# Optimization experiments

Measured on AMD Instinct MI355X. Metric: run time of the kernel, lower is better.

## Reference

```python
import jax, jax.numpy as jnp
import numpy as np

B, S, N = 8, 4, 64
ATOM_FDIM, BOND_FDIM, H = 133, 147, 300
DEPTH = 3


def setup_inputs() -> dict:
    key = jax.random.key(0)
    ks = jax.random.split(key, 9)
    f_atoms = jax.random.normal(ks[0], (B, S, N, ATOM_FDIM), dtype=jnp.float32)
    f_bonds = jax.random.uniform(ks[1], (B, S, N, N, BOND_FDIM), dtype=jnp.float32)
    adj = (jax.random.uniform(ks[2], (B, S, N, N)) < 0.3).astype(jnp.float32)
    def lin(k, fan_in, fan_out):
        return jax.random.normal(k, (fan_in, fan_out), dtype=jnp.float32) / np.sqrt(fan_in)
    return {
        'f_atoms': f_atoms,
        'f_bonds': f_bonds,
        'adj': adj,
        'W_i_atom': lin(ks[3], ATOM_FDIM, H),   # bias=False
        'W_i_bond': lin(ks[4], BOND_FDIM, H),   # bias=False
        'W_h_0': lin(ks[5], H, H),              # bias=False
        'W_h_1': lin(ks[6], H, H),              # bias=False
        'W_o': lin(ks[7], 3 * H, H),            # bias=True
        'b_o': jax.random.normal(ks[8], (H,), dtype=jnp.float32) * 0.01,
    }


def reference(f_atoms, f_bonds, adj, W_i_atom, W_i_bond, W_h_0, W_h_1, W_o, b_o):
    act = jax.nn.relu
    # atom / bond input embeddings
    input_atom = act(f_atoms @ W_i_atom)                        # [B,S,N,H]
    message_atom = input_atom
    input_bond = act((adj[..., None] * f_bonds) @ W_i_bond)     # [B,S,N,N,H]
    message_bond = input_bond
    for W_h in (W_h_0, W_h_1):  # depth-1 message-passing steps
        agg = message_bond.sum(axis=2) * jax.nn.sigmoid(message_bond.max(axis=2))  # [B,S,N,H]
        message_atom = message_atom + agg
        resonance = jnp.einsum('bsnd,bsmd->bsnm', message_atom, message_atom) * adj  # [B,S,N,N]
        # broadcast atom messages along edges, subtract reverse message
        mb = adj[..., None] * message_atom[:, :, None, :, :] - message_bond  # [B,S,N,N,H]
        mb = jnp.swapaxes(mb, 2, 3)  # permute(0,1,3,2,4)
        mb = act(input_bond + mb @ W_h)
        message_bond = mb * jax.nn.softmax(resonance, axis=2)[..., None]
    agg = message_bond.sum(axis=2) * jax.nn.sigmoid(message_bond.max(axis=2))
    a_input = jnp.concatenate([agg, message_atom, input_atom], axis=-1)  # [B,S,N,3H]
    atom_hiddens = act(a_input @ W_o + b_o)  # [B,S,N,H]
    return atom_hiddens, message_bond
```

## Files before the change

kernel.cpp:

```cpp
#include <hip/hip_runtime.h>
#include <hip/hip_bf16.h>
#include <math.h>

#define Bc 8
#define Sc 4
#define Nc 64
#define AF 133
#define BFD 147
#define Hc 300
#define BS (Bc*Sc)
#define ROWS (BS*Nc)
#define EDGES (BS*Nc*Nc)
#define BSLICE 19456
#define BHALF  9728

typedef float f32x4 __attribute__((ext_vector_type(4)));
typedef short bf16x8 __attribute__((ext_vector_type(8)));
typedef float f32x4v __attribute__((ext_vector_type(4)));
typedef f32x4v f32x4u __attribute__((aligned(4)));
union U4 { uint4 u; bf16x8 v; };

__device__ __forceinline__ float reluf(float x){ return fmaxf(x, 0.f); }
__device__ __forceinline__ float b2f(unsigned short u){ union{unsigned int i;float f;}v; v.i = ((unsigned int)u)<<16; return v.f; }
__device__ __forceinline__ unsigned short f2b(float f){ __hip_bfloat16 h = __float2bfloat16(f); return *reinterpret_cast<unsigned short*>(&h); }
__device__ __forceinline__ void split2(float x, unsigned short &hi, unsigned short &lo){
    unsigned short h = f2b(x);
    float r = x - b2f(h);
    hi = h; lo = f2b(r);
}

typedef __attribute__((address_space(1))) const unsigned int* gas1_t;
typedef __attribute__((address_space(3))) unsigned int* las3_t;
__device__ __forceinline__ void gload_lds16(const void* g, void* l){
    __builtin_amdgcn_global_load_lds((gas1_t)g, (las3_t)l, 16, 0, 0);
}

__device__ __forceinline__ void bar_only(){
    __builtin_amdgcn_sched_barrier(0);
    asm volatile("" ::: "memory");
    __builtin_amdgcn_s_barrier();
    asm volatile("" ::: "memory");
    __builtin_amdgcn_sched_barrier(0);
}
__device__ __forceinline__ void bar_drain(){
    __builtin_amdgcn_sched_barrier(0);
    asm volatile("s_waitcnt vmcnt(0) lgkmcnt(0)" ::: "memory");
    __builtin_amdgcn_s_barrier();
    asm volatile("" ::: "memory");
    __builtin_amdgcn_sched_barrier(0);
}

__global__ __launch_bounds__(320) void k_atom_embed(const float* __restrict__ f_atoms,
        const float* __restrict__ W, float* __restrict__ input_atom, float* __restrict__ message_atom){
    __shared__ float x[AF];
    int row = blockIdx.x;
    const float* fr = f_atoms + (size_t)row*AF;
    for (int d = threadIdx.x; d < AF; d += blockDim.x) x[d] = fr[d];
    __syncthreads();
    int h = threadIdx.x;
    if (h < Hc){
        float acc = 0.f;
        for (int d = 0; d < AF; ++d) acc = fmaf(x[d], W[d*Hc + h], acc);
        float v = reluf(acc);
        input_atom[(size_t)row*Hc + h] = v;
        message_atom[(size_t)row*Hc + h] = v;
    }
}

__global__ __launch_bounds__(256) void k_prep_wp2(const float* __restrict__ W, int K, int NKT,
        unsigned short* __restrict__ WP){
    int idx = blockIdx.x*256 + threadIdx.x;
    if (idx >= NKT*BSLICE) return;
    int j  = idx & 7;
    int l  = (idx >> 3) & 63;
    int ct = (idx >> 9) % 19;
    int rem = idx / BHALF;
    int hl = rem & 1;
    int kt = rem >> 1;
    int col = ct*16 + (l & 15);
    int k   = kt*32 + (l >> 4)*8 + j;
    float v = (col < Hc && k < K) ? W[k*Hc + col] : 0.f;
    unsigned short hi, lo; split2(v, hi, lo);
    WP[idx] = hl ? lo : hi;
}

template<int MODE>
__global__ __launch_bounds__(1024) void k_gemm_t(
        const float* __restrict__ Asrc,
        const unsigned short* __restrict__ WP,
        const float* __restrict__ ma,
        const float* __restrict__ adj,
        const float* __restrict__ sm,
        const float* __restrict__ ib,
        float* __restrict__ dst)
{
    constexpr int NKT  = MODE ? 10 : 5;
    constexpr int ASTR = MODE ? 300 : BFD;

    __shared__ unsigned short sAhi[4096];
    __shared__ unsigned short sAlo[4096];
    __shared__ unsigned short sB[BSLICE];
    __shared__ int s_eOut[128];
    __shared__ int s_eRev[128];
    __shared__ float s_adjRev[128];
    __shared__ int s_aAtom[128];

    const int t = threadIdx.x;
    if (MODE){
        if (t < 128){
            int r = t;
            int bs = blockIdx.x >> 5, kk = blockIdx.x & 31;
            int s1 = 64-kk, s2 = 127-2*kk, s3 = 128-kk;
            int a, b;
            if (r < s1){ a = kk; b = kk + r; }
            else if (r < s2){ a = kk+1 + (r - s1); b = kk; }
            else if (r < s3){ a = 63-kk; b = 63-kk + (r - s2); }
            else { a = 64-kk + (r - s3); b = 63-kk; }
            int eo = (bs*64 + a)*64 + b;
            int er = (bs*64 + b)*64 + a;
            s_eOut[r] = eo; s_eRev[r] = er; s_aAtom[r] = bs*64 + a;
            s_adjRev[r] = adj[er];
        }
        __syncthreads();
    }

    const int rt_b = t >> 7;
    const int q_b  = (t >> 5) & 3;
    const int li_b = (t >> 1) & 15;
    const int half = t & 1;
    const int brow = rt_b*16 + li_b;
    const int koff = q_b*8 + 4*half;
    const float* aRow;
    const float* mRow = nullptr;
    float adjR = 0.f;
    if (MODE){
        aRow = Asrc + (size_t)s_eRev[brow]*ASTR;
        mRow = ma + (size_t)s_aAtom[brow]*Hc;
        adjR = s_adjRev[brow];
    } else {
        int e = blockIdx.x*128 + brow;
        aRow = Asrc + (size_t)e*ASTR;
        adjR = adj[e];
    }

    float pm[4], pa[4];
    auto prefetchA = [&](int kt){
        int k0 = kt*32 + koff;
        if (MODE){
            if (k0 <= 296){
                float4 v = *(const float4*)(aRow + k0);
                float4 w = *(const float4*)(mRow + k0);
                pm[0]=v.x; pm[1]=v.y; pm[2]=v.z; pm[3]=v.w;
                pa[0]=w.x; pa[1]=w.y; pa[2]=w.z; pa[3]=w.w;
            }
        } else {
            if (k0 + 3 < BFD){
                f32x4u v = *(const f32x4u*)(aRow + k0);
                pm[0]=v.x; pm[1]=v.y; pm[2]=v.z; pm[3]=v.w;
            } else {
                #pragma unroll
                for (int j = 0; j < 4; ++j){
                    int k = k0 + j;
                    pm[j] = (k < BFD) ? aRow[k] : 0.f;
                }
            }
        }
    };
    auto buildA = [&](int kt){
        int k0 = kt*32 + koff;
        float xv[4];
        if (MODE){
            if (k0 <= 296){
                #pragma unroll
                for (int j = 0; j < 4; ++j) xv[j] = fmaf(adjR, pa[j], -pm[j]);
            } else { xv[0]=xv[1]=xv[2]=xv[3]=0.f; }
        } else {
            #pragma unroll
            for (int j = 0; j < 4; ++j) xv[j] = adjR * pm[j];
        }
        unsigned short h0,l0,h1,l1,h2,l2,h3,l3;
        split2(xv[0],h0,l0); split2(xv[1],h1,l1);
        split2(xv[2],h2,l2); split2(xv[3],h3,l3);
        uint2 hw, lw;
        hw.x = (unsigned int)h0 | ((unsigned int)h1<<16);
        hw.y = (unsigned int)h2 | ((unsigned int)h3<<16);
        lw.x = (unsigned int)l0 | ((unsigned int)l1<<16);
        lw.y = (unsigned int)l2 | ((unsigned int)l3<<16);
        *(uint2*)&sAhi[4*t] = hw;
        *(uint2*)&sAlo[4*t] = lw;
    };
    auto copyB = [&](int kt){
        const unsigned short* src = WP + (size_t)kt*BSLICE;
        #pragma unroll
        for (int rep = 0; rep < 3; ++rep){
            int i = t + rep*1024;
            if (i < BSLICE/8)
                gload_lds16(src + (size_t)i*8, &sB[i*8]);
        }
    };

    const int wv = t >> 6, lane = t & 63;
    const int li = lane & 15, quad = lane >> 4;
    const int rg = wv & 3;
    const int cg = wv >> 2;
    const int c0 = cg*5;
    const int myC = (cg < 3) ? 5 : 4;

    f32x4 acc[5][2];
    #pragma unroll
    for (int c = 0; c < 5; ++c){ acc[c][0] = (f32x4){0,0,0,0}; acc[c][1] = (f32x4){0,0,0,0}; }

    prefetchA(0);

    if (MODE){
        #pragma unroll
        for (int c = 0; c < 5; ++c){
            if (c < myC){
                int h = (c0 + c)*16 + li;
                if (h < Hc){
                    #pragma unroll
                    for (int r2 = 0; r2 < 2; ++r2)
                        #pragma unroll
                        for (int i = 0; i < 4; ++i){
                            int row = (2*rg + r2)*16 + quad*4 + i;
                            acc[c][r2][i] = ib[(size_t)s_eOut[row]*Hc + h];
                        }
                }
            }
        }
    }

    for (int kt = 0; kt < NKT; ++kt){
        if (kt) bar_only();
        copyB(kt);
        buildA(kt);
        bar_drain();
        if (kt+1 < NKT) prefetchA(kt+1);
        __builtin_amdgcn_s_setprio(1);
        U4 a0h, a0l, a1h, a1l;
        a0h.u = *(const uint4*)&sAhi[((2*rg  )*64 + lane)*8];
        a0l.u = *(const uint4*)&sAlo[((2*rg  )*64 + lane)*8];
        a1h.u = *(const uint4*)&sAhi[((2*rg+1)*64 + lane)*8];
        a1l.u = *(const uint4*)&sAlo[((2*rg+1)*64 + lane)*8];
        #pragma unroll
        for (int c = 0; c < 5; ++c){
            if (c < myC){
                U4 bh, bl;
                bh.u = *(const uint4*)&sB[        (c0+c)*512 + lane*8];
                bl.u = *(const uint4*)&sB[BHALF + (c0+c)*512 + lane*8];
                acc[c][0] = __builtin_amdgcn_mfma_f32_16x16x32_bf16(a0h.v, bl.v, acc[c][0], 0,0,0);
                acc[c][0] = __builtin_amdgcn_mfma_f32_16x16x32_bf16(a0l.v, bh.v, acc[c][0], 0,0,0);
                acc[c][0] = __builtin_amdgcn_mfma_f32_16x16x32_bf16(a0h.v, bh.v, acc[c][0], 0,0,0);
                acc[c][1] = __builtin_amdgcn_mfma_f32_16x16x32_bf16(a1h.v, bl.v, acc[c][1], 0,0,0);
                acc[c][1] = __builtin_amdgcn_mfma_f32_16x16x32_bf16(a1l.v, bh.v, acc[c][1], 0,0,0);
                acc[c][1] = __builtin_amdgcn_mfma_f32_16x16x32_bf16(a1h.v, bh.v, acc[c][1], 0,0,0);
            }
        }
        __builtin_amdgcn_s_setprio(0);
    }

    int eO[2][4]; float smv[2][4];
    #pragma unroll
    for (int r2 = 0; r2 < 2; ++r2)
        #pragma unroll
        for (int i = 0; i < 4; ++i){
            int row = (2*rg + r2)*16 + quad*4 + i;
            int e = MODE ? s_eOut[row] : blockIdx.x*128 + row;
            eO[r2][i] = e;
            if (MODE) smv[r2][i] = sm[e];
        }
    #pragma unroll
    for (int c = 0; c < 5; ++c){
        if (c >= myC) continue;
        int h = (c0 + c)*16 + li;
        if (h >= Hc) continue;
        #pragma unroll
        for (int r2 = 0; r2 < 2; ++r2)
            #pragma unroll
            for (int i = 0; i < 4; ++i){
                size_t off = (size_t)eO[r2][i]*Hc + h;
                float v = acc[c][r2][i];
                if (MODE) v = reluf(v) * smv[r2][i];
                else      v = reluf(v);
                dst[off] = v;
            }
    }
}

__global__ __launch_bounds__(320) void k_agg(const float* __restrict__ message_bond,
        float* __restrict__ message_atom, float* __restrict__ agg_out, int final_mode){
    int t = threadIdx.x;
    int r = t / 80, c = t - r*80;
    if (c >= 75) return;
    int row = blockIdx.x*4 + r;
    int bs = row >> 6, m = row & 63;
    size_t base = ((size_t)(bs*Nc)*Nc + m)*(size_t)Hc + (size_t)c*4;
    float4 s  = {0.f, 0.f, 0.f, 0.f};
    float4 mx = {-INFINITY, -INFINITY, -INFINITY, -INFINITY};
    #pragma unroll 4
    for (int n = 0; n < Nc; ++n){
        float4 v = *(const float4*)(message_bond + base + (size_t)n*Nc*Hc);
        s.x += v.x; s.y += v.y; s.z += v.z; s.w += v.w;
        mx.x = fmaxf(mx.x, v.x); mx.y = fmaxf(mx.y, v.y);
        mx.z = fmaxf(mx.z, v.z); mx.w = fmaxf(mx.w, v.w);
    }
    float4 agg;
    agg.x = s.x * (1.f/(1.f + expf(-mx.x)));
    agg.y = s.y * (1.f/(1.f + expf(-mx.y)));
    agg.z = s.z * (1.f/(1.f + expf(-mx.z)));
    agg.w = s.w * (1.f/(1.f + expf(-mx.w)));
    size_t o = (size_t)row*Hc + (size_t)c*4;
    if (final_mode){
        *(float4*)(agg_out + o) = agg;
    } else {
        float4 cur = *(const float4*)(message_atom + o);
        cur.x += agg.x; cur.y += agg.y; cur.z += agg.z; cur.w += agg.w;
        *(float4*)(message_atom + o) = cur;
    }
}

__global__ __launch_bounds__(256) void k_resonance_softmax(const float* __restrict__ message_atom,
        const float* __restrict__ adj, float* __restrict__ sm){
    int bs = blockIdx.x >> 6, m = blockIdx.x & 63;
    __shared__ float am[Hc];
    __shared__ float res[Nc];
    for (int d = threadIdx.x; d < Hc; d += blockDim.x)
        am[d] = message_atom[((size_t)(bs*Nc)+m)*Hc + d];
    __syncthreads();
    int wave = threadIdx.x >> 6, lane = threadIdx.x & 63;
    for (int n = wave; n < Nc; n += 4){
        const float* man = message_atom + ((size_t)(bs*Nc)+n)*Hc;
        float acc = 0.f;
        for (int d = lane; d < Hc; d += 64) acc = fmaf(man[d], am[d], acc);
        #pragma unroll
        for (int off = 32; off > 0; off >>= 1) acc += __shfl_xor(acc, off, 64);
        if (lane == 0) res[n] = acc * adj[((size_t)(bs*Nc)+n)*Nc + m];
    }
    __syncthreads();
    if (threadIdx.x < Nc){
        float v = res[threadIdx.x];
        float mx = v;
        #pragma unroll
        for (int off = 32; off > 0; off >>= 1) mx = fmaxf(mx, __shfl_xor(mx, off, 64));
        float e = expf(v - mx);
        float ssum = e;
        #pragma unroll
        for (int off = 32; off > 0; off >>= 1) ssum += __shfl_xor(ssum, off, 64);
        sm[((size_t)(bs*Nc)+threadIdx.x)*Nc + m] = e / ssum;
    }
}

#define R7 4
__global__ __launch_bounds__(320) void k_output(const float* __restrict__ agg,
        const float* __restrict__ message_atom, const float* __restrict__ input_atom,
        const float* __restrict__ W_o, const float* __restrict__ b_o, float* __restrict__ out){
    __shared__ float xin[R7][3*Hc];
    int r0 = blockIdx.x * R7;
    for (int idx = threadIdx.x; idx < R7*3*Hc; idx += blockDim.x){
        int r = idx / (3*Hc), k = idx - r*(3*Hc);
        int row = r0 + r;
        float v;
        if (k < Hc)           v = agg[(size_t)row*Hc + k];
        else if (k < 2*Hc)    v = message_atom[(size_t)row*Hc + (k - Hc)];
        else                  v = input_atom[(size_t)row*Hc + (k - 2*Hc)];
        xin[r][k] = v;
    }
    __syncthreads();
    int h = threadIdx.x;
    if (h < Hc){
        float acc[R7];
        #pragma unroll
        for (int r=0;r<R7;r++) acc[r] = b_o[h];
        for (int d = 0; d < 3*Hc; ++d){
            float w = W_o[d*Hc + h];
            #pragma unroll
            for (int r=0;r<R7;r++) acc[r] = fmaf(xin[r][d], w, acc[r]);
        }
        #pragma unroll
        for (int r=0;r<R7;r++) out[(size_t)(r0+r)*Hc + h] = reluf(acc[r]);
    }
}

extern "C" void kernel_launch(void* const* d_in, const int* in_sizes, int n_in,
                              void* d_out, int out_size, void* d_ws, size_t ws_size,
                              hipStream_t stream){
    const float* f_atoms  = (const float*)d_in[0];
    const float* f_bonds  = (const float*)d_in[1];
    const float* adj      = (const float*)d_in[2];
    const float* W_i_atom = (const float*)d_in[3];
    const float* W_i_bond = (const float*)d_in[4];
    const float* W_h0     = (const float*)d_in[5];
    const float* W_h1     = (const float*)d_in[6];
    const float* W_o      = (const float*)d_in[7];
    const float* b_o      = (const float*)d_in[8];

    float* out = (float*)d_out;
    float* atom_hiddens = out;
    float* mb_out = out + (size_t)ROWS*Hc;

    float* wsf = (float*)d_ws;
    float* input_atom   = wsf; wsf += (size_t)ROWS*Hc;
    float* message_atom = wsf; wsf += (size_t)ROWS*Hc;
    float* sm           = wsf; wsf += (size_t)EDGES;
    float* ib           = wsf; wsf += (size_t)EDGES*Hc;
    unsigned short* wsu = (unsigned short*)wsf;
    unsigned short* WP0 = wsu; wsu += 10*BSLICE;
    unsigned short* WP1 = wsu; wsu += 10*BSLICE;
    unsigned short* WPb = wsu; wsu += 5*BSLICE;
    float* agg_out = ib;

    k_atom_embed<<<ROWS, 320, 0, stream>>>(f_atoms, W_i_atom, input_atom, message_atom);
    k_prep_wp2<<<(10*BSLICE + 255)/256, 256, 0, stream>>>(W_h0, Hc, 10, WP0);
    k_prep_wp2<<<(10*BSLICE + 255)/256, 256, 0, stream>>>(W_h1, Hc, 10, WP1);
    k_prep_wp2<<<(5*BSLICE + 255)/256, 256, 0, stream>>>(W_i_bond, BFD, 5, WPb);
    k_gemm_t<0><<<EDGES/128, 1024, 0, stream>>>(f_bonds, WPb, nullptr, adj, nullptr, nullptr, ib);
    k_agg<<<ROWS/4, 320, 0, stream>>>(ib, message_atom, nullptr, 0);
    k_resonance_softmax<<<ROWS, 256, 0, stream>>>(message_atom, adj, sm);
    k_gemm_t<1><<<BS*32, 1024, 0, stream>>>(ib, WP0, message_atom, adj, sm, ib, mb_out);
    k_agg<<<ROWS/4, 320, 0, stream>>>(mb_out, message_atom, nullptr, 0);
    k_resonance_softmax<<<ROWS, 256, 0, stream>>>(message_atom, adj, sm);
    k_gemm_t<1><<<BS*32, 1024, 0, stream>>>(mb_out, WP1, message_atom, adj, sm, ib, mb_out);
    k_agg<<<ROWS/4, 320, 0, stream>>>(mb_out, nullptr, agg_out, 1);
    k_output<<<ROWS/R7, 320, 0, stream>>>(agg_out, message_atom, input_atom, W_o, b_o, atom_hiddens);
}
```

Baseline: 756.5 us.

## Fuse neighbor sum/max aggregation into bond GEMM epilogues via column-tiled edge mapping

```diff
diff --git a/kernel.cpp b/kernel.cpp
--- a/kernel.cpp
+++ b/kernel.cpp
@@ -92,10 +92,11 @@
         const float* __restrict__ adj,
         const float* __restrict__ sm,
         const float* __restrict__ ib,
-        float* __restrict__ dst)
+        float* __restrict__ dst,
+        float* __restrict__ aggb)
 {
-    constexpr int NKT  = MODE ? 10 : 5;
-    constexpr int ASTR = MODE ? 300 : BFD;
+    constexpr int NKT  = (MODE != 0) ? 10 : 5;
+    constexpr int ASTR = (MODE != 0) ? 300 : BFD;
 
     __shared__ unsigned short sAhi[4096];
     __shared__ unsigned short sAlo[4096];
@@ -106,7 +107,10 @@
     __shared__ int s_aAtom[128];
 
     const int t = threadIdx.x;
-    if (MODE){
+    const int bs0 = blockIdx.x >> 5;
+    const int mp0 = blockIdx.x & 31;
+
+    if constexpr (MODE == 1){
         if (t < 128){
             int r = t;
             int bs = blockIdx.x >> 5, kk = blockIdx.x & 31;
@@ -133,12 +137,19 @@
     const float* aRow;
     const float* mRow = nullptr;
     float adjR = 0.f;
-    if (MODE){
+    if constexpr (MODE == 1){
         aRow = Asrc + (size_t)s_eRev[brow]*ASTR;
         mRow = ma + (size_t)s_aAtom[brow]*Hc;
         adjR = s_adjRev[brow];
+    } else if constexpr (MODE == 2){
+        int n = brow & 63, cc = brow >> 6;
+        int eR = (bs0*64 + (2*mp0 + cc))*64 + n;
+        aRow = Asrc + (size_t)eR*ASTR;
+        mRow = ma + (size_t)(bs0*64 + n)*Hc;
+        adjR = adj[eR];
     } else {
-        int e = blockIdx.x*128 + brow;
+        int n = brow & 63, cc = brow >> 6;
+        int e = (bs0*64 + n)*64 + (2*mp0 + cc);
         aRow = Asrc + (size_t)e*ASTR;
         adjR = adj[e];
     }
@@ -146,7 +157,7 @@
     float pm[4], pa[4];
     auto prefetchA = [&](int kt){
         int k0 = kt*32 + koff;
-        if (MODE){
+        if constexpr (MODE != 0){
             if (k0 <= 296){
                 float4 v = *(const float4*)(aRow + k0);
                 float4 w = *(const float4*)(mRow + k0);
@@ -169,7 +180,7 @@
     auto buildA = [&](int kt){
         int k0 = kt*32 + koff;
         float xv[4];
-        if (MODE){
+        if constexpr (MODE != 0){
             if (k0 <= 296){
                 #pragma unroll
                 for (int j = 0; j < 4; ++j) xv[j] = fmaf(adjR, pa[j], -pm[j]);
@@ -212,7 +223,7 @@
 
     prefetchA(0);
 
-    if (MODE){
+    if constexpr (MODE != 0){
         #pragma unroll
         for (int c = 0; c < 5; ++c){
             if (c < myC){
@@ -223,7 +234,10 @@
                         #pragma unroll
                         for (int i = 0; i < 4; ++i){
                             int row = (2*rg + r2)*16 + quad*4 + i;
-                            acc[c][r2][i] = ib[(size_t)s_eOut[row]*Hc + h];
+                            int e;
+                            if constexpr (MODE == 1) e = s_eOut[row];
+                            else e = (bs0*64 + (row & 63))*64 + (2*mp0 + (row >> 6));
+                            acc[c][r2][i] = ib[(size_t)e*Hc + h];
                         }
                 }
             }
@@ -259,31 +273,91 @@
         __builtin_amdgcn_s_setprio(0);
     }
 
-    int eO[2][4]; float smv[2][4];
-    #pragma unroll
-    for (int r2 = 0; r2 < 2; ++r2)
-        #pragma unroll
-        for (int i = 0; i < 4; ++i){
-            int row = (2*rg + r2)*16 + quad*4 + i;
-            int e = MODE ? s_eOut[row] : blockIdx.x*128 + row;
-            eO[r2][i] = e;
-            if (MODE) smv[r2][i] = sm[e];
-        }
-    #pragma unroll
-    for (int c = 0; c < 5; ++c){
-        if (c >= myC) continue;
-        int h = (c0 + c)*16 + li;
-        if (h >= Hc) continue;
+    if constexpr (MODE == 1){
+        int eO[2][4]; float smv[2][4];
         #pragma unroll
         for (int r2 = 0; r2 < 2; ++r2)
             #pragma unroll
             for (int i = 0; i < 4; ++i){
-                size_t off = (size_t)eO[r2][i]*Hc + h;
-                float v = acc[c][r2][i];
-                if (MODE) v = reluf(v) * smv[r2][i];
-                else      v = reluf(v);
-                dst[off] = v;
-            }
+                int row = (2*rg + r2)*16 + quad*4 + i;
+                int e = s_eOut[row];
+                eO[r2][i] = e;
+                smv[r2][i] = sm[e];
+            }
+        #pragma unroll
+        for (int c = 0; c < 5; ++c){
+            if (c >= myC) continue;
+            int h = (c0 + c)*16 + li;
+            if (h >= Hc) continue;
+            #pragma unroll
+            for (int r2 = 0; r2 < 2; ++r2)
+                #pragma unroll
+                for (int i = 0; i < 4; ++i){
+                    size_t off = (size_t)eO[r2][i]*Hc + h;
+                    dst[off] = reluf(acc[c][r2][i]) * smv[r2][i];
+                }
+        }
+    } else {
+        __syncthreads();
+        float* sRedS = (float*)sB;
+        float* sRedM = sRedS + 16*304;
+        int eO[2][4]; float smv[2][4];
+        #pragma unroll
+        for (int r2 = 0; r2 < 2; ++r2)
+            #pragma unroll
+            for (int i = 0; i < 4; ++i){
+                int row = (2*rg + r2)*16 + quad*4 + i;
+                int e = (bs0*64 + (row & 63))*64 + (2*mp0 + (row >> 6));
+                eO[r2][i] = e;
+                if constexpr (MODE == 2) smv[r2][i] = sm[e];
+            }
+        #pragma unroll
+        for (int c = 0; c < 5; ++c){
+            float s8 = 0.f, m8 = -INFINITY;
+            int h = (c0 + c)*16 + li;
+            if (c < myC && h < Hc){
+                #pragma unroll
+                for (int r2 = 0; r2 < 2; ++r2)
+                    #pragma unroll
+                    for (int i = 0; i < 4; ++i){
+                        float v = reluf(acc[c][r2][i]);
+                        if constexpr (MODE == 2) v *= smv[r2][i];
+                        dst[(size_t)eO[r2][i]*Hc + h] = v;
+                        s8 += v; m8 = fmaxf(m8, v);
+                    }
+            }
+            s8 += __shfl_xor(s8, 16, 64); s8 += __shfl_xor(s8, 32, 64);
+            m8 = fmaxf(m8, __shfl_xor(m8, 16, 64)); m8 = fmaxf(m8, __shfl_xor(m8, 32, 64));
+            if (c < myC && quad == 0){
+                sRedS[wv*304 + (c0 + c)*16 + li] = s8;
+                sRedM[wv*304 + (c0 + c)*16 + li] = m8;
+            }
+        }
+        __syncthreads();
+        if (t < 608){
+            int cc = t / 304, h = t - cc*304;
+            if (h < Hc){
+                int ct = h >> 4;
+                int cgf = (ct < 15) ? (ct/5) : 3;
+                int w0 = (cgf << 2) + 2*cc;
+                float s = sRedS[w0*304 + h] + sRedS[(w0+1)*304 + h];
+                float m = fmaxf(sRedM[w0*304 + h], sRedM[(w0+1)*304 + h]);
+                float agg = s * (1.f/(1.f + expf(-m)));
+                size_t o = (size_t)(bs0*64 + 2*mp0 + cc)*Hc + h;
+                if constexpr (MODE == 0) aggb[o] += agg;
+                else                     aggb[o]  = agg;
+            }
+        }
+    }
+}
+
+__global__ __launch_bounds__(256) void k_ma_add(float* __restrict__ ma, const float* __restrict__ aggb){
+    int i = blockIdx.x*256 + threadIdx.x;
+    if (i < ROWS*Hc/4){
+        float4 a = ((const float4*)aggb)[i];
+        float4 v = ((float4*)ma)[i];
+        v.x += a.x; v.y += a.y; v.z += a.z; v.w += a.w;
+        ((float4*)ma)[i] = v;
     }
 }
 
@@ -402,6 +476,7 @@
     float* input_atom   = wsf; wsf += (size_t)ROWS*Hc;
     float* message_atom = wsf; wsf += (size_t)ROWS*Hc;
     float* sm           = wsf; wsf += (size_t)EDGES;
+    float* aggb         = wsf; wsf += (size_t)ROWS*Hc;
     float* ib           = wsf; wsf += (size_t)EDGES*Hc;
     unsigned short* wsu = (unsigned short*)wsf;
     unsigned short* WP0 = wsu; wsu += 10*BSLICE;
@@ -413,13 +488,12 @@
     k_prep_wp2<<<(10*BSLICE + 255)/256, 256, 0, stream>>>(W_h0, Hc, 10, WP0);
     k_prep_wp2<<<(10*BSLICE + 255)/256, 256, 0, stream>>>(W_h1, Hc, 10, WP1);
     k_prep_wp2<<<(5*BSLICE + 255)/256, 256, 0, stream>>>(W_i_bond, BFD, 5, WPb);
-    k_gemm_t<0><<<EDGES/128, 1024, 0, stream>>>(f_bonds, WPb, nullptr, adj, nullptr, nullptr, ib);
-    k_agg<<<ROWS/4, 320, 0, stream>>>(ib, message_atom, nullptr, 0);
+    k_gemm_t<0><<<BS*32, 1024, 0, stream>>>(f_bonds, WPb, nullptr, adj, nullptr, nullptr, ib, message_atom);
     k_resonance_softmax<<<ROWS, 256, 0, stream>>>(message_atom, adj, sm);
-    k_gemm_t<1><<<BS*32, 1024, 0, stream>>>(ib, WP0, message_atom, adj, sm, ib, mb_out);
-    k_agg<<<ROWS/4, 320, 0, stream>>>(mb_out, message_atom, nullptr, 0);
+    k_gemm_t<2><<<BS*32, 1024, 0, stream>>>(ib, WP0, message_atom, adj, sm, ib, mb_out, aggb);
+    k_ma_add<<<(ROWS*Hc/4 + 255)/256, 256, 0, stream>>>(message_atom, aggb);
     k_resonance_softmax<<<ROWS, 256, 0, stream>>>(message_atom, adj, sm);
-    k_gemm_t<1><<<BS*32, 1024, 0, stream>>>(mb_out, WP1, message_atom, adj, sm, ib, mb_out);
+    k_gemm_t<1><<<BS*32, 1024, 0, stream>>>(mb_out, WP1, message_atom, adj, sm, ib, mb_out, nullptr);
     k_agg<<<ROWS/4, 320, 0, stream>>>(mb_out, nullptr, agg_out, 1);
     k_output<<<ROWS/R7, 320, 0, stream>>>(agg_out, message_atom, input_atom, W_o, b_o, atom_hiddens);
 }
```

New measurement: 754.1 us. No clear change (-0.3%).
